# Optimization experiments

Measured on AMD Instinct MI355X. Metric: run time of the kernel, lower is better.

Reference implementation:

```python
import jax, jax.numpy as jnp
import numpy as np


def gcn_conv(x, src, dst, W, b, N):
    """PyG GCNConv: add self-loops, symmetric D^-1/2 (A+I) D^-1/2 normalization."""
    loop = jnp.arange(N, dtype=src.dtype)
    s = jnp.concatenate([src, loop])
    d = jnp.concatenate([dst, loop])
    deg = jnp.zeros((N,), dtype=x.dtype).at[d].add(1.0)  # in-degree incl. self-loop
    dinv = jax.lax.rsqrt(deg)  # deg >= 1 because of self-loops
    norm = dinv[s] * dinv[d]  # [E+N]
    h = x @ W  # [N, out] linear transform first (as in PyG)
    msg = h[s] * norm[:, None]  # gather + scale
    out = jax.ops.segment_sum(msg, d, num_segments=N)  # scatter-add
    return out + b


def setup_inputs() -> dict:
    key = jax.random.key(0)
    ks = jax.random.split(key, 10)
    N, E, in_dim, h1, h2, A = 100000, 3200000, 256, 32, 64, 64
    x = jax.random.normal(ks[0], (N, in_dim), dtype=jnp.float32)
    ei = jax.random.randint(ks[1], (2, E), 0, N, dtype=jnp.int64)
    def glorot(k, shape):
        lim = float(np.sqrt(6.0 / (shape[0] + shape[1])))
        return jax.random.uniform(k, shape, jnp.float32, -lim, lim)
    return {
        "x": x,
        "ei": ei,
        "num_nodes": N,
        "W1": glorot(ks[2], (in_dim, h1)), "b1": jnp.zeros((h1,), jnp.float32),
        "W2": glorot(ks[3], (h1, h2)),     "b2": jnp.zeros((h2,), jnp.float32),
        "Wo1": glorot(ks[4], (h2, h2)),    "bo1": jnp.zeros((h2,), jnp.float32),
        "Wo2": glorot(ks[5], (h2, A)),     "bo2": jnp.zeros((A,), jnp.float32),
    }


def reference(x, ei, num_nodes, W1, b1, W2, b2, Wo1, bo1, Wo2, bo2):
    src, dst = ei[0], ei[1]
    z = jax.nn.relu(gcn_conv(x, src, dst, W1, b1, num_nodes))
    z = jax.nn.relu(gcn_conv(z, src, dst, W2, b2, num_nodes))
    logits = jax.nn.relu(z @ Wo1 + bo1) @ Wo2 + bo2  # [N, action_space]
    nbatches = z.shape[0] // num_nodes
    # original reshapes with z.size(1)=hidden2 (== action_space here)
    dist = logits.reshape(nbatches, num_nodes * z.shape[1])
    return jax.nn.softmax(dist, axis=-1)  # Categorical probs
```

## Files before the change

kernel.cpp:

```cpp
#include <hip/hip_runtime.h>

#define DEVI __device__ __forceinline__

DEVI unsigned fkey(float f) {
  unsigned u = __float_as_uint(f);
  return u ^ ((u >> 31) ? 0xFFFFFFFFu : 0x80000000u);
}
DEVI float funkey(unsigned k) {
  unsigned b = (k & 0x80000000u) ? (k ^ 0x80000000u) : ~k;
  return __uint_as_float(b);
}
DEVI float f4get(const float4& v, int j) {
  return j == 0 ? v.x : j == 1 ? v.y : j == 2 ? v.z : v.w;
}

constexpr int BSH = 9;
constexpr int BNODES = 1 << BSH;
constexpr int PEPT = 16;
constexpr int PCHUNK = 256 * PEPT;

__global__ void k_binit(int* __restrict__ bcnt) {
  bcnt[threadIdx.x] = 0;
}

__global__ void k_bcount(const int* __restrict__ dst, int* __restrict__ bcnt,
                         int E, int NB) {
  __shared__ int lh[256];
  lh[threadIdx.x] = 0;
  __syncthreads();
  int stride = gridDim.x * 256;
  for (long i = (long)blockIdx.x * 256 + threadIdx.x; i < E; i += stride)
    atomicAdd(&lh[dst[i] >> BSH], 1);
  __syncthreads();
  if (threadIdx.x < NB && lh[threadIdx.x]) atomicAdd(&bcnt[threadIdx.x], lh[threadIdx.x]);
}

__global__ void k_bscan(const int* __restrict__ bcnt, int* __restrict__ bbase,
                        int* __restrict__ bcur, unsigned* __restrict__ scal, int NB) {
  __shared__ int s[256];
  int t = threadIdx.x;
  int v = (t < NB) ? bcnt[t] : 0;
  s[t] = v;
  __syncthreads();
  for (int o = 1; o < 256; o <<= 1) {
    int add = (t >= o) ? s[t - o] : 0;
    __syncthreads();
    s[t] += add;
    __syncthreads();
  }
  int excl = s[t] - v;
  if (t < NB) { bbase[t] = excl; bcur[t] = excl; }
  if (t == 0) { scal[0] = 0u; scal[1] = 0u; }
}

__global__ __launch_bounds__(256)
void k_bpart(const int* __restrict__ src, const int* __restrict__ dst,
             int* __restrict__ bcur, unsigned* __restrict__ epart, int E, int NB) {
  __shared__ int lh[256];
  __shared__ int gbase[256];
  long base = (long)blockIdx.x * PCHUNK;
  lh[threadIdx.x] = 0;
  __syncthreads();
  int ed[PEPT]; int es[PEPT]; unsigned short lpos[PEPT];
#pragma unroll
  for (int j = 0; j < PEPT; j++) {
    long i = base + threadIdx.x + (long)j * 256;
    if (i < E) {
      int d = dst[i];
      es[j] = src[i];
      ed[j] = d;
      lpos[j] = (unsigned short)atomicAdd(&lh[d >> BSH], 1);
    } else {
      ed[j] = -1;
    }
  }
  __syncthreads();
  if (threadIdx.x < NB) {
    int c = lh[threadIdx.x];
    gbase[threadIdx.x] = c ? atomicAdd(&bcur[threadIdx.x], c) : 0;
  }
  __syncthreads();
#pragma unroll
  for (int j = 0; j < PEPT; j++) {
    int d = ed[j];
    if (d >= 0) {
      unsigned p = (unsigned)(gbase[d >> BSH] + (int)lpos[j]);
      epart[p] = ((unsigned)(d & (BNODES - 1)) << 17) | (unsigned)es[j];
    }
  }
}

__global__ __launch_bounds__(256)
void k_fine(const unsigned* __restrict__ epart, const int* __restrict__ bbase,
            const int* __restrict__ bcnt, int* __restrict__ rowptr,
            int* __restrict__ deg, float* __restrict__ dinv,
            int* __restrict__ col, int N) {
  __shared__ int lh[BNODES];
  __shared__ int lexcl[BNODES];
  __shared__ int ssc[256];
  int b = blockIdx.x;
  int base = bbase[b], cnt = bcnt[b];
  int nlo = b << BSH;
  int t = threadIdx.x;
  lh[t] = 0; lh[t + 256] = 0;
  __syncthreads();
  for (int i = t; i < cnt; i += 256) {
    unsigned e = epart[base + i];
    atomicAdd(&lh[e >> 17], 1);
  }
  __syncthreads();
  int a0 = lh[2 * t], a1 = lh[2 * t + 1];
  ssc[t] = a0 + a1;
  __syncthreads();
  for (int o = 1; o < 256; o <<= 1) {
    int add = (t >= o) ? ssc[t - o] : 0;
    __syncthreads();
    ssc[t] += add;
    __syncthreads();
  }
  int excl = ssc[t] - (a0 + a1);
  lexcl[2 * t] = excl;
  lexcl[2 * t + 1] = excl + a0;
  __syncthreads();
#pragma unroll
  for (int k = 0; k < 2; k++) {
    int i = t + k * 256;
    int v = nlo + i;
    if (v < N) {
      int dgv = lh[i];
      deg[v] = dgv;
      rowptr[v] = base + lexcl[i];
      dinv[v] = rsqrtf((float)(dgv + 1));
    }
  }
  __syncthreads();
  lh[2 * t] = lexcl[2 * t];
  lh[2 * t + 1] = lexcl[2 * t + 1];
  __syncthreads();
  for (int i = t; i < cnt; i += 256) {
    unsigned e = epart[base + i];
    int p = atomicAdd(&lh[e >> 17], 1);
    col[base + p] = (int)(e & 0x1FFFFu);
  }
}

__global__ __launch_bounds__(256)
void k_gemm1(const float* __restrict__ in, const float* __restrict__ W,
             const float* __restrict__ dinv, float* __restrict__ out, int N) {
  __shared__ float Wl[256 * 32];
  {
    const float4* W4 = (const float4*)W;
    float4* Wl4 = (float4*)Wl;
    for (int i = threadIdx.x; i < 256 * 32 / 4; i += 256) Wl4[i] = W4[i];
  }
  __syncthreads();

  int t = threadIdx.x;
  int cg = t & 7;
  int rg = t >> 3;
  int c0 = cg * 4;
  long r0 = (long)blockIdx.x * 128 + rg * 4;

  bool rv[4];
#pragma unroll
  for (int i = 0; i < 4; i++) rv[i] = (r0 + i) < (long)N;

  const float* ip = in + r0 * 256;

  float acc[4][4];
#pragma unroll
  for (int i = 0; i < 4; i++)
#pragma unroll
    for (int c = 0; c < 4; c++) acc[i][c] = 0.f;

#pragma unroll 2
  for (int k = 0; k < 256; k += 4) {
    float4 xv[4];
#pragma unroll
    for (int i = 0; i < 4; i++)
      xv[i] = rv[i] ? *(const float4*)(ip + (long)i * 256 + k)
                    : make_float4(0.f, 0.f, 0.f, 0.f);
#pragma unroll
    for (int jj = 0; jj < 4; jj++) {
      const float4 w = *(const float4*)&Wl[(k + jj) * 32 + c0];
#pragma unroll
      for (int i = 0; i < 4; i++) {
        float xs = f4get(xv[i], jj);
        acc[i][0] = fmaf(xs, w.x, acc[i][0]);
        acc[i][1] = fmaf(xs, w.y, acc[i][1]);
        acc[i][2] = fmaf(xs, w.z, acc[i][2]);
        acc[i][3] = fmaf(xs, w.w, acc[i][3]);
      }
    }
  }

#pragma unroll
  for (int i = 0; i < 4; i++) {
    if (!rv[i]) continue;
    float dv = dinv[r0 + i];
    float* op = &out[(r0 + i) * 32 + c0];
    *(float4*)op = make_float4(acc[i][0] * dv, acc[i][1] * dv,
                               acc[i][2] * dv, acc[i][3] * dv);
  }
}

template <int K, int COLS, int ROWS, bool BIAS, bool RELU, bool SCALE, bool DOMAX>
__launch_bounds__(256)
__global__ void k_gemm(const float* __restrict__ in, const float* __restrict__ W,
                       const float* __restrict__ bias, const float* __restrict__ dinv,
                       float* __restrict__ out, int N, unsigned* __restrict__ gmax) {
  constexpr int CG = COLS / 8;
  constexpr int RG = 256 / CG;
  constexpr int RPB = RG * ROWS;
  __shared__ float Wl[K * COLS];
  for (int i = threadIdx.x; i < K * COLS; i += 256) Wl[i] = W[i];
  __syncthreads();

  int cg = threadIdx.x % CG, rg = threadIdx.x / CG;
  int c0 = cg * 8;
  long r0 = (long)blockIdx.x * RPB + rg * ROWS;

  float acc[ROWS][8];
#pragma unroll
  for (int i = 0; i < ROWS; i++)
#pragma unroll
    for (int c = 0; c < 8; c++) acc[i][c] = 0.f;
  bool rv[ROWS];
#pragma unroll
  for (int i = 0; i < ROWS; i++) rv[i] = (r0 + i) < (long)N;

  const float* ip = in + r0 * K;
#pragma unroll 2
  for (int k = 0; k < K; k += 4) {
    float4 xv[ROWS];
#pragma unroll
    for (int i = 0; i < ROWS; i++)
      xv[i] = rv[i] ? *(const float4*)(ip + (long)i * K + k) : make_float4(0.f, 0.f, 0.f, 0.f);
#pragma unroll
    for (int jj = 0; jj < 4; jj++) {
      const float4 wa = *(const float4*)&Wl[(k + jj) * COLS + c0];
      const float4 wb = *(const float4*)&Wl[(k + jj) * COLS + c0 + 4];
#pragma unroll
      for (int i = 0; i < ROWS; i++) {
        float xs = f4get(xv[i], jj);
        acc[i][0] = fmaf(xs, wa.x, acc[i][0]);
        acc[i][1] = fmaf(xs, wa.y, acc[i][1]);
        acc[i][2] = fmaf(xs, wa.z, acc[i][2]);
        acc[i][3] = fmaf(xs, wa.w, acc[i][3]);
        acc[i][4] = fmaf(xs, wb.x, acc[i][4]);
        acc[i][5] = fmaf(xs, wb.y, acc[i][5]);
        acc[i][6] = fmaf(xs, wb.z, acc[i][6]);
        acc[i][7] = fmaf(xs, wb.w, acc[i][7]);
      }
    }
  }

  float bo[8];
  if (BIAS) {
#pragma unroll
    for (int c = 0; c < 8; c++) bo[c] = bias[c0 + c];
  }
  float m = -3.4e38f;
#pragma unroll
  for (int i = 0; i < ROWS; i++) {
    if (!rv[i]) continue;
    float dv = SCALE ? dinv[r0 + i] : 1.f;
    float o[8];
#pragma unroll
    for (int c = 0; c < 8; c++) {
      float v = acc[i][c];
      if (BIAS) v += bo[c];
      if (SCALE) v *= dv;
      if (RELU) v = fmaxf(v, 0.f);
      if (DOMAX) m = fmaxf(m, v);
      o[c] = v;
    }
    float* op = &out[(r0 + i) * COLS + c0];
    *(float4*)(op) = make_float4(o[0], o[1], o[2], o[3]);
    *(float4*)(op + 4) = make_float4(o[4], o[5], o[6], o[7]);
  }
  if constexpr (DOMAX) {
    __shared__ float red[256];
    red[threadIdx.x] = m;
    __syncthreads();
    for (int o = 128; o > 0; o >>= 1) {
      if (threadIdx.x < o) red[threadIdx.x] = fmaxf(red[threadIdx.x], red[threadIdx.x + o]);
      __syncthreads();
    }
    if (threadIdx.x == 0) atomicMax(gmax, fkey(red[0]));
  }
}

template <int FEAT, bool BIAS, bool RELU, bool PSCALE>
__launch_bounds__(256)
__global__ void k_aggv(const float* __restrict__ g, const int* __restrict__ col,
                       const int* __restrict__ rowptr, const int* __restrict__ deg,
                       const float* __restrict__ dinv, const float* __restrict__ bias,
                       float* __restrict__ out, int N) {
  constexpr int LPN = FEAT / 4;
  constexpr int NPB = 256 / LPN;
  int nib = threadIdx.x / LPN;
  int c = threadIdx.x % LPN;
  long v = (long)blockIdx.x * NPB + nib;
  if (v >= N) return;

  const float4* g4 = (const float4*)g;
  float4 acc = g4[v * LPN + c];
  int start = rowptr[v], dg = deg[v];
  int e = 0;
  while (e < dg) {
    int cnt = min(LPN, dg - e);
    int idx = (c < cnt) ? col[start + e + c] : 0;
    int j = 0;
    for (; j + 4 <= cnt; j += 4) {
      int u0 = __shfl(idx, j + 0, LPN);
      int u1 = __shfl(idx, j + 1, LPN);
      int u2 = __shfl(idx, j + 2, LPN);
      int u3 = __shfl(idx, j + 3, LPN);
      float4 a0 = g4[(long)u0 * LPN + c];
      float4 a1 = g4[(long)u1 * LPN + c];
      float4 a2 = g4[(long)u2 * LPN + c];
      float4 a3 = g4[(long)u3 * LPN + c];
      acc.x += (a0.x + a1.x) + (a2.x + a3.x);
      acc.y += (a0.y + a1.y) + (a2.y + a3.y);
      acc.z += (a0.z + a1.z) + (a2.z + a3.z);
      acc.w += (a0.w + a1.w) + (a2.w + a3.w);
    }
    for (; j < cnt; j++) {
      int u = __shfl(idx, j, LPN);
      float4 a = g4[(long)u * LPN + c];
      acc.x += a.x; acc.y += a.y; acc.z += a.z; acc.w += a.w;
    }
    e += cnt;
  }
  float dv = dinv[v];
  float4 val;
  val.x = acc.x * dv; val.y = acc.y * dv; val.z = acc.z * dv; val.w = acc.w * dv;
  if (BIAS) {
    float4 b = ((const float4*)bias)[c];
    val.x += b.x; val.y += b.y; val.z += b.z; val.w += b.w;
  }
  if (RELU) {
    val.x = fmaxf(val.x, 0.f); val.y = fmaxf(val.y, 0.f);
    val.z = fmaxf(val.z, 0.f); val.w = fmaxf(val.w, 0.f);
  }
  if (PSCALE) {
    val.x *= dv; val.y *= dv; val.z *= dv; val.w *= dv;
  }
  ((float4*)out)[v * LPN + c] = val;
}

__global__ void k_smsum(const float* __restrict__ logit, unsigned* __restrict__ scal, int total) {
  __shared__ float s[256];
  float gmax = funkey(scal[0]);
  float loc = 0.f;
  for (int i = blockIdx.x * 256 + threadIdx.x; i < total; i += gridDim.x * 256)
    loc += expf(logit[i] - gmax);
  s[threadIdx.x] = loc; __syncthreads();
  for (int o = 128; o > 0; o >>= 1) {
    if (threadIdx.x < o) s[threadIdx.x] += s[threadIdx.x + o];
    __syncthreads();
  }
  if (threadIdx.x == 0) atomicAdd((float*)&scal[1], s[0]);
}

__global__ void k_smnorm(float* __restrict__ logit, const unsigned* __restrict__ scal, int total) {
  float gmax = funkey(scal[0]);
  float inv = 1.0f / __uint_as_float(scal[1]);
  int i = blockIdx.x * 256 + threadIdx.x;
  if (i < total) logit[i] = expf(logit[i] - gmax) * inv;
}

extern "C" void kernel_launch(void* const* d_in, const int* in_sizes, int n_in,
                              void* d_out, int out_size, void* d_ws, size_t ws_size,
                              hipStream_t stream) {
  const float* x   = (const float*)d_in[0];
  const int*   ei  = (const int*)d_in[1];
  const float* W1  = (const float*)d_in[3];
  const float* b1  = (const float*)d_in[4];
  const float* W2  = (const float*)d_in[5];
  const float* b2  = (const float*)d_in[6];
  const float* Wo1 = (const float*)d_in[7];
  const float* bo1 = (const float*)d_in[8];
  const float* Wo2 = (const float*)d_in[9];
  const float* bo2 = (const float*)d_in[10];

  const int N = in_sizes[0] / 256;
  const int E = in_sizes[1] / 2;
  const int* src = ei;
  const int* dst = ei + E;
  const int NB = (N + BNODES - 1) / BNODES;

  size_t o = 0;
  auto carve = [&](size_t bytes) -> char* {
    char* p = (char*)d_ws + o;
    o += (bytes + 255) & ~(size_t)255;
    return p;
  };
  float* R1     = (float*)carve((size_t)N * 64 * 4);
  float* R2     = (float*)carve((size_t)N * 64 * 4);
  int*   col    = (int*)carve((size_t)E * 4);
  int*   deg    = (int*)carve((size_t)N * 4);
  float* dinv   = (float*)carve((size_t)N * 4);
  int*   rowptr = (int*)carve((size_t)N * 4);
  int*   bcnt   = (int*)carve(256 * 4);
  int*   bbase  = (int*)carve(256 * 4);
  int*   bcur   = (int*)carve(256 * 4);
  unsigned* scal = (unsigned*)carve(64);

  unsigned* epart = (unsigned*)R2;
  float* g1 = R1;
  float* p  = R2;
  float* s2 = R1;
  float* z2 = R2;
  float* t  = R1;
  float* logits = (float*)d_out;

  k_binit<<<1, 256, 0, stream>>>(bcnt);
  k_bcount<<<512, 256, 0, stream>>>(dst, bcnt, E, NB);
  k_bscan<<<1, 256, 0, stream>>>(bcnt, bbase, bcur, scal, NB);
  k_bpart<<<(E + PCHUNK - 1) / PCHUNK, 256, 0, stream>>>(src, dst, bcur, epart, E, NB);
  k_fine<<<NB, 256, 0, stream>>>(epart, bbase, bcnt, rowptr, deg, dinv, col, N);

  const int g1G = (N + 127) / 128;
  const int gG = (N + 63) / 64;
  const int gA = (N + 31) / 32;

  k_gemm1<<<g1G, 256, 0, stream>>>(x, W1, dinv, g1, N);
  k_aggv<32, true, true, true><<<gA, 256, 0, stream>>>(g1, col, rowptr, deg, dinv, b1, p, N);

  k_aggv<32, false, false, false><<<gA, 256, 0, stream>>>(p, col, rowptr, deg, dinv, nullptr, s2, N);
  k_gemm<32, 64, 2, true, true, false, false>
      <<<gG, 256, 0, stream>>>(s2, W2, b2, nullptr, z2, N, nullptr);

  k_gemm<64, 64, 2, true, true, false, false>
      <<<gG, 256, 0, stream>>>(z2, Wo1, bo1, nullptr, t, N, nullptr);
  k_gemm<64, 64, 2, true, false, false, true>
      <<<gG, 256, 0, stream>>>(t, Wo2, bo2, nullptr, logits, N, scal);

  k_smsum<<<1024, 256, 0, stream>>>(logits, scal, out_size);
  k_smnorm<<<(out_size + 255) / 256, 256, 0, stream>>>(logits, scal, out_size);
}
```

Baseline: 574.7 us.

## Stage x tiles through double-buffered swizzled LDS in first GEMM

```diff
diff --git a/kernel.cpp b/kernel.cpp
--- a/kernel.cpp
+++ b/kernel.cpp
@@ -148,59 +148,100 @@
 void k_gemm1(const float* __restrict__ in, const float* __restrict__ W,
              const float* __restrict__ dinv, float* __restrict__ out, int N) {
   __shared__ float Wl[256 * 32];
+  __shared__ float xb[2][128 * 16];
+  const int t = threadIdx.x;
+
   {
     const float4* W4 = (const float4*)W;
     float4* Wl4 = (float4*)Wl;
-    for (int i = threadIdx.x; i < 256 * 32 / 4; i += 256) Wl4[i] = W4[i];
-  }
-  __syncthreads();
-
-  int t = threadIdx.x;
-  int cg = t & 7;
-  int rg = t >> 3;
-  int c0 = cg * 4;
-  long r0 = (long)blockIdx.x * 128 + rg * 4;
-
-  bool rv[4];
-#pragma unroll
-  for (int i = 0; i < 4; i++) rv[i] = (r0 + i) < (long)N;
-
-  const float* ip = in + r0 * 256;
-
-  float acc[4][4];
-#pragma unroll
-  for (int i = 0; i < 4; i++)
-#pragma unroll
-    for (int c = 0; c < 4; c++) acc[i][c] = 0.f;
-
-#pragma unroll 2
-  for (int k = 0; k < 256; k += 4) {
-    float4 xv[4];
-#pragma unroll
-    for (int i = 0; i < 4; i++)
-      xv[i] = rv[i] ? *(const float4*)(ip + (long)i * 256 + k)
-                    : make_float4(0.f, 0.f, 0.f, 0.f);
-#pragma unroll
-    for (int jj = 0; jj < 4; jj++) {
-      const float4 w = *(const float4*)&Wl[(k + jj) * 32 + c0];
-#pragma unroll
-      for (int i = 0; i < 4; i++) {
-        float xs = f4get(xv[i], jj);
-        acc[i][0] = fmaf(xs, w.x, acc[i][0]);
-        acc[i][1] = fmaf(xs, w.y, acc[i][1]);
-        acc[i][2] = fmaf(xs, w.z, acc[i][2]);
-        acc[i][3] = fmaf(xs, w.w, acc[i][3]);
+#pragma unroll
+    for (int i = 0; i < 8; i++) Wl4[t + i * 256] = W4[t + i * 256];
+  }
+
+  const int srow = t >> 1;
+  const int part = t & 1;
+  const int sk = (srow >> 1) & 3;
+  long grow = (long)blockIdx.x * 128 + srow;
+  const float* gsrc = in + (grow < (long)N ? grow : (long)(N - 1)) * 256 + part * 8;
+  const int q0 = part * 2, q1 = part * 2 + 1;
+  const int ws0 = srow * 16 + ((q0 ^ sk) << 2);
+  const int ws1 = srow * 16 + ((q1 ^ sk) << 2);
+
+  const int cg = t & 3;
+  const int rg = t >> 2;
+  const int c0 = cg * 8;
+  const int rk = (rg >> 1) & 3;
+
+  {
+    float4 a = *(const float4*)(gsrc + 0);
+    float4 b = *(const float4*)(gsrc + 4);
+    *(float4*)&xb[0][ws0] = a;
+    *(float4*)&xb[0][ws1] = b;
+  }
+  __syncthreads();
+
+  float acc[2][8];
+#pragma unroll
+  for (int i = 0; i < 2; i++)
+#pragma unroll
+    for (int c = 0; c < 8; c++) acc[i][c] = 0.f;
+
+  for (int ch = 0; ch < 16; ch++) {
+    float4 na, nb;
+    if (ch < 15) {
+      na = *(const float4*)(gsrc + (ch + 1) * 16 + 0);
+      nb = *(const float4*)(gsrc + (ch + 1) * 16 + 4);
+    }
+    const float* xc = xb[ch & 1];
+#pragma unroll
+    for (int q = 0; q < 4; q++) {
+      float4 xv0 = *(const float4*)&xc[rg * 16 + ((q ^ rk) << 2)];
+      float4 xv1 = *(const float4*)&xc[(rg + 64) * 16 + ((q ^ rk) << 2)];
+#pragma unroll
+      for (int jj = 0; jj < 4; jj++) {
+        const float* wr = &Wl[(ch * 16 + q * 4 + jj) * 32 + c0];
+        float4 wa = *(const float4*)(wr);
+        float4 wb = *(const float4*)(wr + 4);
+        float x0 = f4get(xv0, jj);
+        float x1 = f4get(xv1, jj);
+        acc[0][0] = fmaf(x0, wa.x, acc[0][0]);
+        acc[0][1] = fmaf(x0, wa.y, acc[0][1]);
+        acc[0][2] = fmaf(x0, wa.z, acc[0][2]);
+        acc[0][3] = fmaf(x0, wa.w, acc[0][3]);
+        acc[0][4] = fmaf(x0, wb.x, acc[0][4]);
+        acc[0][5] = fmaf(x0, wb.y, acc[0][5]);
+        acc[0][6] = fmaf(x0, wb.z, acc[0][6]);
+        acc[0][7] = fmaf(x0, wb.w, acc[0][7]);
+        acc[1][0] = fmaf(x1, wa.x, acc[1][0]);
+        acc[1][1] = fmaf(x1, wa.y, acc[1][1]);
+        acc[1][2] = fmaf(x1, wa.z, acc[1][2]);
+        acc[1][3] = fmaf(x1, wa.w, acc[1][3]);
+        acc[1][4] = fmaf(x1, wb.x, acc[1][4]);
+        acc[1][5] = fmaf(x1, wb.y, acc[1][5]);
+        acc[1][6] = fmaf(x1, wb.z, acc[1][6]);
+        acc[1][7] = fmaf(x1, wb.w, acc[1][7]);
       }
     }
-  }
-
-#pragma unroll
-  for (int i = 0; i < 4; i++) {
-    if (!rv[i]) continue;
-    float dv = dinv[r0 + i];
-    float* op = &out[(r0 + i) * 32 + c0];
-    *(float4*)op = make_float4(acc[i][0] * dv, acc[i][1] * dv,
-                               acc[i][2] * dv, acc[i][3] * dv);
+    if (ch < 15) {
+      __syncthreads();
+      float* xn = xb[(ch + 1) & 1];
+      *(float4*)&xn[ws0] = na;
+      *(float4*)&xn[ws1] = nb;
+      __syncthreads();
+    }
+  }
+
+#pragma unroll
+  for (int i = 0; i < 2; i++) {
+    long r = (long)blockIdx.x * 128 + rg + i * 64;
+    if (r < (long)N) {
+      float dv = dinv[r];
+      float* op = &out[r * 32 + c0];
+      *(float4*)(op) = make_float4(acc[i][0] * dv, acc[i][1] * dv,
+                                   acc[i][2] * dv, acc[i][3] * dv);
+      *(float4*)(op + 4) = make_float4(acc[i][4] * dv, acc[i][5] * dv,
+                                       acc[i][6] * dv, acc[i][7] * dv);
+    }
   }
 }
 
```

Result: faster. 517.6 us (-9.9%).
